# Optimization experiments

Hardware: AMD Instinct MI355X
Metric: run time of the kernel (lower is better)

Reference implementation:

```python
import jax, jax.numpy as jnp
import numpy as np

B, C, O, H, W, KH, KW = 8, 32, 64, 64, 64, 3, 3
K = KH * KW
PAD = 1


def setup_inputs() -> dict:
    key = jax.random.key(0)
    k1, k2 = jax.random.split(key)
    x = jax.random.normal(k1, (B, C, H, W), dtype=jnp.float32)
    # unshared locally-connected weights, scaled like the torch init
    weight = jax.random.normal(k2, (1, O, C, H, W, K), dtype=jnp.float32) / np.sqrt(C * K)
    return {"x": x, "weight": weight}


def reference(x, weight):
    # Extract 3x3 patches (same order as torch unfold: per-channel, row-major kh,kw)
    # patches: [B, C*K, H, W] with channel-major ordering (c, kh, kw)
    patches = jax.lax.conv_general_dilated_patches(
        x, filter_shape=(KH, KW), window_strides=(1, 1), padding=[(PAD, PAD), (PAD, PAD)]
    )
    patches = patches.reshape(B, C, K, H, W)
    # out[b,o,h,w] = sum_{c,k} patches[b,c,k,h,w] * weight[0,o,c,h,w,k]
    out = jnp.einsum('bckhw,ochwk->bohw', patches, weight[0])
    return out
```

## Files before the change

### kernel.cpp

```cpp
#include <hip/hip_runtime.h>


#define BB 8
#define CC 32
#define OO 64
#define HH 64
#define WW 64
#define KK 9
#define CHW (CC * HH * WW)
#define OHW (HH * WW)
#define WCS (HH * WW * KK)
#define WOS (CC * HH * WW * KK)

__global__ __launch_bounds__(256, 2)
void lc2d_kernel(const float* __restrict__ x,
                 const float* __restrict__ wgt,
                 float* __restrict__ out)
{
  const int tid  = threadIdx.x;
  const int w    = tid & 63;
  const int osub = tid >> 6;
  const int h    = blockIdx.x & 63;
  const int og   = blockIdx.x >> 6;
  const int o0   = og * 8 + osub * 2;

  __shared__ float4 xs[2][2][198];

  const int p   = tid;
  const int dh  = (p >= 132) ? 2 : ((p >= 66) ? 1 : 0);
  const int wpp = p - dh * 66;
  const int r   = h + dh - 1;
  const int col = wpp - 1;
  const bool sactive = (p < 198);
  const bool svalid  = sactive && (r >= 0) && (r < HH) && (col >= 0) && (col < WW);
  const int xoff0 = r * WW + col;

  const float* wq0 = wgt + (o0 * CC * HH + h) * (WW * KK) + w * KK;
  const float* wq1 = wq0 + WOS;

  float acc[2][8];
#pragma unroll
  for (int j = 0; j < 2; ++j)
#pragma unroll
    for (int b = 0; b < 8; ++b) acc[j][b] = 0.f;

  auto load_stage = [&](int c, float4& lo, float4& hi) {
    lo = make_float4(0.f, 0.f, 0.f, 0.f);
    hi = make_float4(0.f, 0.f, 0.f, 0.f);
    if (svalid) {
      const float* q = x + (xoff0 + c * OHW);
      lo.x = q[0 * CHW]; lo.y = q[1 * CHW]; lo.z = q[2 * CHW]; lo.w = q[3 * CHW];
      hi.x = q[4 * CHW]; hi.y = q[5 * CHW]; hi.z = q[6 * CHW]; hi.w = q[7 * CHW];
    }
  };

  auto load_w = [&](int c, float (&wrr)[2][KK]) {
    const float* a = wq0 + c * WCS;
    const float* b = wq1 + c * WCS;
#pragma unroll
    for (int k = 0; k < KK; ++k) { wrr[0][k] = a[k]; wrr[1][k] = b[k]; }
  };

  auto compute = [&](int cur, const float (&wrr)[2][KK]) {
    float4 plo[KK], phi[KK];
#pragma unroll
    for (int d = 0; d < 3; ++d)
#pragma unroll
      for (int e = 0; e < 3; ++e) {
        plo[d * 3 + e] = xs[cur][0][d * 66 + w + e];
        phi[d * 3 + e] = xs[cur][1][d * 66 + w + e];
      }
#pragma unroll
    for (int k = 0; k < KK; ++k) {
      float xf[8];
      xf[0] = plo[k].x; xf[1] = plo[k].y; xf[2] = plo[k].z; xf[3] = plo[k].w;
      xf[4] = phi[k].x; xf[5] = phi[k].y; xf[6] = phi[k].z; xf[7] = phi[k].w;
#pragma unroll
      for (int j = 0; j < 2; ++j) {
        const float wf = wrr[j][k];
#pragma unroll
        for (int b = 0; b < 8; ++b)
          acc[j][b] = fmaf(wf, xf[b], acc[j][b]);
      }
    }
  };

  float4 slo, shi;
  load_stage(0, slo, shi);
  float wr[2][KK];
  load_w(0, wr);
  if (sactive) { xs[0][0][p] = slo; xs[0][1][p] = shi; }
  __syncthreads();

  for (int c = 0; c < CC - 1; ++c) {
    float4 nlo, nhi;
    load_stage(c + 1, nlo, nhi);
    float wn[2][KK];
    load_w(c + 1, wn);

    compute(c & 1, wr);

    if (sactive) { xs[(c + 1) & 1][0][p] = nlo; xs[(c + 1) & 1][1][p] = nhi; }
#pragma unroll
    for (int k = 0; k < KK; ++k) { wr[0][k] = wn[0][k]; wr[1][k] = wn[1][k]; }
    __syncthreads();
  }
  compute((CC - 1) & 1, wr);

#pragma unroll
  for (int j = 0; j < 2; ++j) {
    const int o = o0 + j;
#pragma unroll
    for (int b = 0; b < 8; ++b)
      out[((b * OO + o) * HH + h) * WW + w] = acc[j][b];
  }
}

extern "C" void kernel_launch(void* const* d_in, const int* in_sizes, int n_in,
                              void* d_out, int out_size, void* d_ws, size_t ws_size,
                              hipStream_t stream) {
  const float* x   = (const float*)d_in[0];
  const float* wgt = (const float*)d_in[1];
  float* out       = (float*)d_out;
  (void)in_sizes; (void)n_in; (void)out_size; (void)d_ws; (void)ws_size;
  lc2d_kernel<<<dim3(HH * (OO / 8)), dim3(256), 0, stream>>>(x, wgt, out);
}
```

Baseline: 405.5 us.

## Stage weight rows through LDS with coalesced float4 loads

Weight loading changes from each thread reading its own 9 strided floats per output channel to the block cooperatively loading the contiguous 8x576-float weight rows for the current channel as float4 into a double-buffered shared-memory array. Each thread then reads its 18 weights from LDS. The goal is coalesced, vectorized global reads of the dominant weight stream. The cost is about 37KB of extra LDS per block, which may reduce occupancy, plus LDS bank conflicts from the stride-9 reads.

```diff
diff --git a/kernel.cpp b/kernel.cpp
--- a/kernel.cpp
+++ b/kernel.cpp
@@ -11,6 +11,7 @@
 #define OHW (HH * WW)
 #define WCS (HH * WW * KK)
 #define WOS (CC * HH * WW * KK)
+#define WROW (WW * KK)
 
 __global__ __launch_bounds__(256, 2)
 void lc2d_kernel(const float* __restrict__ x,
@@ -25,6 +26,7 @@
   const int o0   = og * 8 + osub * 2;
 
   __shared__ float4 xs[2][2][198];
+  __shared__ float wsh[2][8 * WROW];
 
   const int p   = tid;
   const int dh  = (p >= 132) ? 2 : ((p >= 66) ? 1 : 0);
@@ -35,8 +37,9 @@
   const bool svalid  = sactive && (r >= 0) && (r < HH) && (col >= 0) && (col < WW);
   const int xoff0 = r * WW + col;
 
-  const float* wq0 = wgt + (o0 * CC * HH + h) * (WW * KK) + w * KK;
-  const float* wq1 = wq0 + WOS;
+  const int soi = tid >> 5;
+  const int sl  = tid & 31;
+  const float* wchunk = wgt + (og * 8 + soi) * WOS + h * WROW;
 
   float acc[2][8];
 #pragma unroll
@@ -54,14 +57,28 @@
     }
   };
 
-  auto load_w = [&](int c, float (&wrr)[2][KK]) {
-    const float* a = wq0 + c * WCS;
-    const float* b = wq1 + c * WCS;
+  auto load_wstage = [&](int c, float4 (&wv)[5]) {
+    const float4* src = reinterpret_cast<const float4*>(wchunk + c * WCS);
 #pragma unroll
-    for (int k = 0; k < KK; ++k) { wrr[0][k] = a[k]; wrr[1][k] = b[k]; }
+    for (int jj = 0; jj < 4; ++jj) wv[jj] = src[sl + 32 * jj];
+    if (sl < 16) wv[4] = src[sl + 128];
   };
 
-  auto compute = [&](int cur, const float (&wrr)[2][KK]) {
+  auto store_wstage = [&](int buf, const float4 (&wv)[5]) {
+    float4* dst = reinterpret_cast<float4*>(&wsh[buf][0]) + soi * 144;
+#pragma unroll
+    for (int jj = 0; jj < 4; ++jj) dst[sl + 32 * jj] = wv[jj];
+    if (sl < 16) dst[sl + 128] = wv[4];
+  };
+
+  auto compute = [&](int cur) {
+    const float* wp = &wsh[cur][(osub * 2) * WROW + w * KK];
+    float wrr[2][KK];
+#pragma unroll
+    for (int k = 0; k < KK; ++k) {
+      wrr[0][k] = wp[k];
+      wrr[1][k] = wp[WROW + k];
+    }
     float4 plo[KK], phi[KK];
 #pragma unroll
     for (int d = 0; d < 3; ++d)
@@ -86,26 +103,26 @@
   };
 
   float4 slo, shi;
+  float4 wv[5];
   load_stage(0, slo, shi);
-  float wr[2][KK];
-  load_w(0, wr);
+  load_wstage(0, wv);
   if (sactive) { xs[0][0][p] = slo; xs[0][1][p] = shi; }
+  store_wstage(0, wv);
   __syncthreads();
 
   for (int c = 0; c < CC - 1; ++c) {
     float4 nlo, nhi;
+    float4 nwv[5];
     load_stage(c + 1, nlo, nhi);
-    float wn[2][KK];
-    load_w(c + 1, wn);
+    load_wstage(c + 1, nwv);
 
-    compute(c & 1, wr);
+    compute(c & 1);
 
     if (sactive) { xs[(c + 1) & 1][0][p] = nlo; xs[(c + 1) & 1][1][p] = nhi; }
-#pragma unroll
-    for (int k = 0; k < KK; ++k) { wr[0][k] = wn[0][k]; wr[1][k] = wn[1][k]; }
+    store_wstage((c + 1) & 1, nwv);
     __syncthreads();
   }
-  compute((CC - 1) & 1, wr);
+  compute((CC - 1) & 1);
 
 #pragma unroll
   for (int j = 0; j < 2; ++j) {
```

Measured after the change: 450.2 us. 1.11x slower.
